# Performance work log

Measured on AMD Instinct MI355X. Metric: run time of the kernel, lower is better.

## Reference

```python
import jax, jax.numpy as jnp
import numpy as np

B = 1048576
EPS = 1e-5

def _lin_params(key, din, dout):
    k1, k2 = jax.random.split(key)
    bound = 1.0 / np.sqrt(din)
    w = jax.random.uniform(k1, (din, dout), minval=-bound, maxval=bound, dtype=jnp.float32)
    b = jax.random.uniform(k2, (dout,), minval=-bound, maxval=bound, dtype=jnp.float32)
    return w, b

def setup_inputs() -> dict:
    key = jax.random.key(0)
    ks = jax.random.split(key, 10)
    x = jax.random.normal(ks[0], (B, 8), dtype=jnp.float32)
    dims = [(8, 16), (16, 16), (16, 12), (12, 8), (8, 4), (4, 4), (4, 4), (4, 1)]
    names = ['fm', 'c1', 'p1', 'c2', 'p2', 'c3', 'r', 'h']
    inp = {'x': x,
           'bn_g': jnp.ones((8,), jnp.float32),
           'bn_b': jnp.zeros((8,), jnp.float32)}
    for i, (nm, (di, do)) in enumerate(zip(names, dims)):
        w, b = _lin_params(ks[i + 1], di, do)
        inp['w_' + nm] = w
        inp['b_' + nm] = b
    return inp

def reference(x, bn_g, bn_b, w_fm, b_fm, w_c1, b_c1, w_p1, b_p1, w_c2, b_c2,
              w_p2, b_p2, w_c3, b_c3, w_r, b_r, w_h, b_h):
    # BatchNorm1d (training mode): batch statistics, biased variance
    mu = jnp.mean(x, axis=0)
    var = jnp.mean((x - mu) ** 2, axis=0)
    h = (x - mu) * jax.lax.rsqrt(var + EPS) * bn_g + bn_b
    h = jnp.tanh(h @ w_fm + b_fm)   # [B,16] feature_map
    h = jnp.tanh(h @ w_c1 + b_c1)   # [B,16] conv1
    h = jnp.tanh(h @ w_p1 + b_p1)   # [B,12] pool1
    h = jnp.tanh(h @ w_c2 + b_c2)   # [B,8]  conv2
    h = jnp.tanh(h @ w_p2 + b_p2)   # [B,4]  pool2
    h = jnp.tanh(h @ w_c3 + b_c3)   # [B,4]  conv3
    res = jax.nn.relu(h @ w_r + b_r)  # [B,4] residual branch
    h = h + res
    return jax.nn.sigmoid(h @ w_h + b_h)  # [B,1]
```

## Files before the change

kernel.cpp:

```cpp
#include <hip/hip_runtime.h>
#include <stdint.h>

#define B_ROWS 1048576
#define STAT_BLOCKS 512
#define MAIN_BLOCKS 2048

typedef __fp16 h2 __attribute__((ext_vector_type(2)));

#define PART_OFF 16
#define WPK_OFF 8208
#define BIA_OFF 8578
#define W_FM 0
#define W_C1 64
#define W_P1 192
#define W_C2 288
#define W_P2 336
#define W_C3 352
#define W_R  360
#define W_H  368
#define B_FM 0
#define B_C1 16
#define B_P1 32
#define B_C2 44
#define B_P2 52
#define B_C3 56
#define B_R  60
#define B_H  64

__device__ __forceinline__ float exp_tanh(float x) {
    float e = __builtin_amdgcn_exp2f(x * 2.8853900817779268f);
    return 1.0f - 2.0f * __builtin_amdgcn_rcpf(e + 1.0f);
}

__device__ __forceinline__ float fast_sigmoid(float x) {
    float e = __builtin_amdgcn_exp2f(x * -1.4426950408889634f);
    return __builtin_amdgcn_rcpf(1.0f + e);
}

template<int DIN, int DOUT>
__device__ void pack_layer(const float* __restrict__ w, const float* __restrict__ b,
                           uint32_t* __restrict__ wdst, float* __restrict__ bdst) {
    for (int idx = threadIdx.x; idx < DOUT * (DIN / 2); idx += blockDim.x) {
        int j = idx / (DIN / 2), i2 = idx % (DIN / 2);
        h2 h;
        h.x = (__fp16)w[(2 * i2) * DOUT + j];
        h.y = (__fp16)w[(2 * i2 + 1) * DOUT + j];
        wdst[j * (DIN / 2) + i2] = __builtin_bit_cast(uint32_t, h);
    }
    for (int j = threadIdx.x; j < DOUT; j += blockDim.x) bdst[j] = b[j];
}

__global__ __launch_bounds__(256) void bn_stats(
    const float* __restrict__ x, float* __restrict__ ws,
    const float* __restrict__ w_fm, const float* __restrict__ b_fm,
    const float* __restrict__ w_c1, const float* __restrict__ b_c1,
    const float* __restrict__ w_p1, const float* __restrict__ b_p1,
    const float* __restrict__ w_c2, const float* __restrict__ b_c2,
    const float* __restrict__ w_p2, const float* __restrict__ b_p2,
    const float* __restrict__ w_c3, const float* __restrict__ b_c3,
    const float* __restrict__ w_r,  const float* __restrict__ b_r,
    const float* __restrict__ w_h,  const float* __restrict__ b_h)
{
    const int tid = blockIdx.x * 256 + threadIdx.x;
    float s[8], q[8];
#pragma unroll
    for (int c = 0; c < 8; ++c) { s[c] = 0.f; q[c] = 0.f; }
    const float4* x4 = (const float4*)x;
#pragma unroll
    for (int k = 0; k < 8; ++k) {
        int r = tid + k * 131072;
        float4 a = x4[2 * r];
        float4 b = x4[2 * r + 1];
        s[0] += a.x; s[1] += a.y; s[2] += a.z; s[3] += a.w;
        s[4] += b.x; s[5] += b.y; s[6] += b.z; s[7] += b.w;
        q[0] += a.x * a.x; q[1] += a.y * a.y; q[2] += a.z * a.z; q[3] += a.w * a.w;
        q[4] += b.x * b.x; q[5] += b.y * b.y; q[6] += b.z * b.z; q[7] += b.w * b.w;
    }
#pragma unroll
    for (int off = 32; off > 0; off >>= 1) {
#pragma unroll
        for (int c = 0; c < 8; ++c) {
            s[c] += __shfl_down(s[c], off);
            q[c] += __shfl_down(q[c], off);
        }
    }
    __shared__ float red[4][16];
    const int lane = threadIdx.x & 63;
    const int wave = threadIdx.x >> 6;
    if (lane == 0) {
#pragma unroll
        for (int c = 0; c < 8; ++c) { red[wave][c] = s[c]; red[wave][8 + c] = q[c]; }
    }
    __syncthreads();
    if (threadIdx.x < 16) {
        float acc = red[0][threadIdx.x] + red[1][threadIdx.x] +
                    red[2][threadIdx.x] + red[3][threadIdx.x];
        ws[PART_OFF + blockIdx.x * 16 + threadIdx.x] = acc;
    }
    if (blockIdx.x == 0) {
        uint32_t* wpk = (uint32_t*)(ws + WPK_OFF);
        float*    bpk = ws + BIA_OFF;
        pack_layer<8, 16>(w_fm, b_fm, wpk + W_FM, bpk + B_FM);
        pack_layer<16,16>(w_c1, b_c1, wpk + W_C1, bpk + B_C1);
        pack_layer<16,12>(w_p1, b_p1, wpk + W_P1, bpk + B_P1);
        pack_layer<12, 8>(w_c2, b_c2, wpk + W_C2, bpk + B_C2);
        pack_layer<8,  4>(w_p2, b_p2, wpk + W_P2, bpk + B_P2);
        pack_layer<4,  4>(w_c3, b_c3, wpk + W_C3, bpk + B_C3);
        pack_layer<4,  4>(w_r,  b_r,  wpk + W_R,  bpk + B_R);
        pack_layer<4,  1>(w_h,  b_h,  wpk + W_H,  bpk + B_H);
    }
}

__global__ __launch_bounds__(256) void bn_finalize(
    const float* __restrict__ bn_g, const float* __restrict__ bn_b,
    float* __restrict__ ws)
{
    __shared__ float accs[16][17];
    const int f = threadIdx.x & 15;
    const int chunk = threadIdx.x >> 4;
    const float* p = ws + PART_OFF + (chunk * 32) * 16 + f;
    float a = 0.f;
#pragma unroll 8
    for (int b = 0; b < 32; ++b) a += p[b * 16];
    accs[chunk][f] = a;
    __syncthreads();
    if (threadIdx.x < 16) {
        float t = 0.f;
#pragma unroll
        for (int c = 0; c < 16; ++c) t += accs[c][threadIdx.x];
        accs[0][threadIdx.x] = t;
    }
    __syncthreads();
    if (threadIdx.x < 8) {
        const float invB = 1.0f / (float)B_ROWS;
        int c = threadIdx.x;
        float mu  = accs[0][c] * invB;
        float var = fmaf(-mu, mu, accs[0][8 + c] * invB);
        float sv  = bn_g[c] * rsqrtf(var + 1e-5f);
        ws[c]     = sv;
        ws[8 + c] = fmaf(-mu, sv, bn_b[c]);
    }
}

__device__ __forceinline__ uint32_t lut_idx(float x) {
    float t = fmaf(x, 1024.0f, 4096.0f);
    t = __builtin_amdgcn_fmed3f(t, 0.0f, 8191.0f);
    return (uint32_t)t;
}

template<int DIN, int DOUT>
__device__ __forceinline__ void layer_dot1(const h2* __restrict__ apk,
                                           float* __restrict__ o,
                                           const uint32_t* __restrict__ wpk,
                                           const float* __restrict__ bias) {
#pragma unroll
    for (int j = 0; j < DOUT; ++j) {
        float acc = bias[j];
#pragma unroll
        for (int i2 = 0; i2 < DIN / 2; ++i2) {
            h2 w = __builtin_bit_cast(h2, wpk[j * (DIN / 2) + i2]);
            acc = __builtin_amdgcn_fdot2(apk[i2], w, acc, false);
        }
        o[j] = acc;
    }
}

template<int N>
__device__ __forceinline__ void tanh_pack1(const float* __restrict__ in,
                                           h2* __restrict__ pk,
                                           const uint16_t* __restrict__ lut16) {
#pragma unroll
    for (int k = 0; k < N / 2; ++k) {
        uint32_t v0 = lut16[lut_idx(in[2 * k])];
        uint32_t v1 = lut16[lut_idx(in[2 * k + 1])];
        pk[k] = __builtin_bit_cast(h2, v0 | (v1 << 16));
    }
}

__device__ __forceinline__ float row_forward(float4 x0, float4 x1,
        const float* __restrict__ sc, const float* __restrict__ sh,
        const uint32_t* __restrict__ wpk, const float* __restrict__ bpk,
        const uint16_t* __restrict__ lut16) {
    float n[8];
    n[0] = fmaf(x0.x, sc[0], sh[0]); n[1] = fmaf(x0.y, sc[1], sh[1]);
    n[2] = fmaf(x0.z, sc[2], sh[2]); n[3] = fmaf(x0.w, sc[3], sh[3]);
    n[4] = fmaf(x1.x, sc[4], sh[4]); n[5] = fmaf(x1.y, sc[5], sh[5]);
    n[6] = fmaf(x1.z, sc[6], sh[6]); n[7] = fmaf(x1.w, sc[7], sh[7]);
    h2 a[4];
#pragma unroll
    for (int k = 0; k < 4; ++k)
        a[k] = __builtin_amdgcn_cvt_pkrtz(n[2 * k], n[2 * k + 1]);

    float o1[16]; h2 p1[8];
    layer_dot1<8, 16>(a, o1, wpk + W_FM, bpk + B_FM);
    tanh_pack1<16>(o1, p1, lut16);
    float o2[16]; h2 p2[8];
    layer_dot1<16,16>(p1, o2, wpk + W_C1, bpk + B_C1);
    tanh_pack1<16>(o2, p2, lut16);
    float o3[12]; h2 p3[6];
    layer_dot1<16,12>(p2, o3, wpk + W_P1, bpk + B_P1);
    tanh_pack1<12>(o3, p3, lut16);
    float o4[8]; h2 p4[4];
    layer_dot1<12, 8>(p3, o4, wpk + W_C2, bpk + B_C2);
    tanh_pack1<8>(o4, p4, lut16);
    float o5[4]; h2 p5[2];
    layer_dot1<8,  4>(p4, o5, wpk + W_P2, bpk + B_P2);
    tanh_pack1<4>(o5, p5, lut16);
    float c4[4];
    layer_dot1<4,  4>(p5, c4, wpk + W_C3, bpk + B_C3);

    uint32_t u[4]; float f[4];
#pragma unroll
    for (int j = 0; j < 4; ++j) {
        u[j] = lut16[lut_idx(c4[j])];
        f[j] = (float)__builtin_bit_cast(__fp16, (uint16_t)u[j]);
    }
    h2 pc[2];
    pc[0] = __builtin_bit_cast(h2, u[0] | (u[1] << 16));
    pc[1] = __builtin_bit_cast(h2, u[2] | (u[3] << 16));
    float r4[4];
    layer_dot1<4,  4>(pc, r4, wpk + W_R, bpk + B_R);
#pragma unroll
    for (int j = 0; j < 4; ++j) f[j] += fmaxf(r4[j], 0.f);
    h2 ph[2];
    ph[0] = __builtin_amdgcn_cvt_pkrtz(f[0], f[1]);
    ph[1] = __builtin_amdgcn_cvt_pkrtz(f[2], f[3]);
    float oh[1];
    layer_dot1<4,  1>(ph, oh, wpk + W_H, bpk + B_H);
    return fast_sigmoid(oh[0]);
}

__global__ __launch_bounds__(256, 6) void qcnn_main(
    const float* __restrict__ x, const float* __restrict__ ws,
    float* __restrict__ out)
{
    const int tid = blockIdx.x * 256 + threadIdx.x;
    const int r0 = tid, r1 = tid + (B_ROWS / 2);
    const float4* x4 = (const float4*)x;
    float4 xa0 = x4[2 * r0], xa1 = x4[2 * r0 + 1];
    float4 xb0 = x4[2 * r1], xb1 = x4[2 * r1 + 1];

    __shared__ uint16_t lut16[8192];
    {
        const float h = 0.0009765625f;
        uint32_t* l32 = (uint32_t*)lut16;
#pragma unroll
        for (int k = 0; k < 16; ++k) {
            int i2 = threadIdx.x + k * 256;
            float c0 = fmaf((float)(2 * i2) + 0.5f, h, -4.0f);
            float c1 = fmaf((float)(2 * i2 + 1) + 0.5f, h, -4.0f);
            __fp16 h0 = (__fp16)exp_tanh(c0);
            __fp16 h1 = (__fp16)exp_tanh(c1);
            l32[i2] = (uint32_t)__builtin_bit_cast(uint16_t, h0)
                    | ((uint32_t)__builtin_bit_cast(uint16_t, h1) << 16);
        }
    }
    float sc[8], sh[8];
#pragma unroll
    for (int c = 0; c < 8; ++c) { sc[c] = ws[c]; sh[c] = ws[8 + c]; }
    __syncthreads();

    const uint32_t* wpk = (const uint32_t*)(ws + WPK_OFF);
    const float*    bpk = ws + BIA_OFF;

    out[r0] = row_forward(xa0, xa1, sc, sh, wpk, bpk, lut16);
    out[r1] = row_forward(xb0, xb1, sc, sh, wpk, bpk, lut16);
}

extern "C" void kernel_launch(void* const* d_in, const int* in_sizes, int n_in,
                              void* d_out, int out_size, void* d_ws, size_t ws_size,
                              hipStream_t stream) {
    const float* x    = (const float*)d_in[0];
    const float* bn_g = (const float*)d_in[1];
    const float* bn_b = (const float*)d_in[2];
    const float* w_fm = (const float*)d_in[3];
    const float* b_fm = (const float*)d_in[4];
    const float* w_c1 = (const float*)d_in[5];
    const float* b_c1 = (const float*)d_in[6];
    const float* w_p1 = (const float*)d_in[7];
    const float* b_p1 = (const float*)d_in[8];
    const float* w_c2 = (const float*)d_in[9];
    const float* b_c2 = (const float*)d_in[10];
    const float* w_p2 = (const float*)d_in[11];
    const float* b_p2 = (const float*)d_in[12];
    const float* w_c3 = (const float*)d_in[13];
    const float* b_c3 = (const float*)d_in[14];
    const float* w_r  = (const float*)d_in[15];
    const float* b_r  = (const float*)d_in[16];
    const float* w_h  = (const float*)d_in[17];
    const float* b_h  = (const float*)d_in[18];
    float* out = (float*)d_out;
    float* ws  = (float*)d_ws;

    bn_stats<<<STAT_BLOCKS, 256, 0, stream>>>(
        x, ws, w_fm, b_fm, w_c1, b_c1, w_p1, b_p1, w_c2, b_c2,
        w_p2, b_p2, w_c3, b_c3, w_r, b_r, w_h, b_h);
    bn_finalize<<<1, 256, 0, stream>>>(bn_g, bn_b, ws);
    qcnn_main<<<MAIN_BLOCKS, 256, 0, stream>>>(x, ws, out);
}
```

Before: 141.0 us.

## Fold batchnorm into first layer weights and replace tanh LUT with direct exp

Folds the batchnorm scale and shift into the first linear layer's packed fp16 weights and bias inside the finalize kernel, so the main kernel skips the per-row normalization FMAs. It also drops the 8192-entry shared-memory tanh lookup table, whose per-block construction, LDS use and syncthreads are removed, and computes tanh directly with exp_tanh plus packed conversion. This trades LDS gathers and table setup for more ALU transcendental work per activation, and raw x is now cast to fp16 before the scaled weights are applied, which changes rounding.

```diff
diff --git a/kernel.cpp b/kernel.cpp
--- a/kernel.cpp
+++ b/kernel.cpp
@@ -52,7 +52,6 @@
 
 __global__ __launch_bounds__(256) void bn_stats(
     const float* __restrict__ x, float* __restrict__ ws,
-    const float* __restrict__ w_fm, const float* __restrict__ b_fm,
     const float* __restrict__ w_c1, const float* __restrict__ b_c1,
     const float* __restrict__ w_p1, const float* __restrict__ b_p1,
     const float* __restrict__ w_c2, const float* __restrict__ b_c2,
@@ -100,7 +99,6 @@
     if (blockIdx.x == 0) {
         uint32_t* wpk = (uint32_t*)(ws + WPK_OFF);
         float*    bpk = ws + BIA_OFF;
-        pack_layer<8, 16>(w_fm, b_fm, wpk + W_FM, bpk + B_FM);
         pack_layer<16,16>(w_c1, b_c1, wpk + W_C1, bpk + B_C1);
         pack_layer<16,12>(w_p1, b_p1, wpk + W_P1, bpk + B_P1);
         pack_layer<12, 8>(w_c2, b_c2, wpk + W_C2, bpk + B_C2);
@@ -113,9 +111,11 @@
 
 __global__ __launch_bounds__(256) void bn_finalize(
     const float* __restrict__ bn_g, const float* __restrict__ bn_b,
+    const float* __restrict__ w_fm, const float* __restrict__ b_fm,
     float* __restrict__ ws)
 {
     __shared__ float accs[16][17];
+    __shared__ float scs[8], shs[8];
     const int f = threadIdx.x & 15;
     const int chunk = threadIdx.x >> 4;
     const float* p = ws + PART_OFF + (chunk * 32) * 16 + f;
@@ -137,15 +137,24 @@
         float mu  = accs[0][c] * invB;
         float var = fmaf(-mu, mu, accs[0][8 + c] * invB);
         float sv  = bn_g[c] * rsqrtf(var + 1e-5f);
-        ws[c]     = sv;
-        ws[8 + c] = fmaf(-mu, sv, bn_b[c]);
-    }
-}
-
-__device__ __forceinline__ uint32_t lut_idx(float x) {
-    float t = fmaf(x, 1024.0f, 4096.0f);
-    t = __builtin_amdgcn_fmed3f(t, 0.0f, 8191.0f);
-    return (uint32_t)t;
+        scs[c] = sv;
+        shs[c] = fmaf(-mu, sv, bn_b[c]);
+    }
+    __syncthreads();
+    if (threadIdx.x < 64) {
+        int j = threadIdx.x >> 2, i2 = threadIdx.x & 3;
+        h2 h;
+        h.x = (__fp16)(w_fm[(2 * i2) * 16 + j]     * scs[2 * i2]);
+        h.y = (__fp16)(w_fm[(2 * i2 + 1) * 16 + j] * scs[2 * i2 + 1]);
+        ((uint32_t*)(ws + WPK_OFF))[W_FM + j * 4 + i2] = __builtin_bit_cast(uint32_t, h);
+    }
+    if (threadIdx.x < 16) {
+        int j = threadIdx.x;
+        float acc = b_fm[j];
+#pragma unroll
+        for (int i = 0; i < 8; ++i) acc = fmaf(shs[i], w_fm[i * 16 + j], acc);
+        (ws + BIA_OFF)[B_FM + j] = acc;
+    }
 }
 
 template<int DIN, int DOUT>
@@ -167,57 +176,47 @@
 
 template<int N>
 __device__ __forceinline__ void tanh_pack1(const float* __restrict__ in,
-                                           h2* __restrict__ pk,
-                                           const uint16_t* __restrict__ lut16) {
+                                           h2* __restrict__ pk) {
 #pragma unroll
     for (int k = 0; k < N / 2; ++k) {
-        uint32_t v0 = lut16[lut_idx(in[2 * k])];
-        uint32_t v1 = lut16[lut_idx(in[2 * k + 1])];
-        pk[k] = __builtin_bit_cast(h2, v0 | (v1 << 16));
+        float t0 = exp_tanh(in[2 * k]);
+        float t1 = exp_tanh(in[2 * k + 1]);
+        pk[k] = __builtin_amdgcn_cvt_pkrtz(t0, t1);
     }
 }
 
 __device__ __forceinline__ float row_forward(float4 x0, float4 x1,
-        const float* __restrict__ sc, const float* __restrict__ sh,
-        const uint32_t* __restrict__ wpk, const float* __restrict__ bpk,
-        const uint16_t* __restrict__ lut16) {
-    float n[8];
-    n[0] = fmaf(x0.x, sc[0], sh[0]); n[1] = fmaf(x0.y, sc[1], sh[1]);
-    n[2] = fmaf(x0.z, sc[2], sh[2]); n[3] = fmaf(x0.w, sc[3], sh[3]);
-    n[4] = fmaf(x1.x, sc[4], sh[4]); n[5] = fmaf(x1.y, sc[5], sh[5]);
-    n[6] = fmaf(x1.z, sc[6], sh[6]); n[7] = fmaf(x1.w, sc[7], sh[7]);
+        const uint32_t* __restrict__ wpk, const float* __restrict__ bpk) {
     h2 a[4];
-#pragma unroll
-    for (int k = 0; k < 4; ++k)
-        a[k] = __builtin_amdgcn_cvt_pkrtz(n[2 * k], n[2 * k + 1]);
+    a[0] = __builtin_amdgcn_cvt_pkrtz(x0.x, x0.y);
+    a[1] = __builtin_amdgcn_cvt_pkrtz(x0.z, x0.w);
+    a[2] = __builtin_amdgcn_cvt_pkrtz(x1.x, x1.y);
+    a[3] = __builtin_amdgcn_cvt_pkrtz(x1.z, x1.w);
 
     float o1[16]; h2 p1[8];
     layer_dot1<8, 16>(a, o1, wpk + W_FM, bpk + B_FM);
-    tanh_pack1<16>(o1, p1, lut16);
+    tanh_pack1<16>(o1, p1);
     float o2[16]; h2 p2[8];
     layer_dot1<16,16>(p1, o2, wpk + W_C1, bpk + B_C1);
-    tanh_pack1<16>(o2, p2, lut16);
+    tanh_pack1<16>(o2, p2);
     float o3[12]; h2 p3[6];
     layer_dot1<16,12>(p2, o3, wpk + W_P1, bpk + B_P1);
-    tanh_pack1<12>(o3, p3, lut16);
+    tanh_pack1<12>(o3, p3);
     float o4[8]; h2 p4[4];
     layer_dot1<12, 8>(p3, o4, wpk + W_C2, bpk + B_C2);
-    tanh_pack1<8>(o4, p4, lut16);
+    tanh_pack1<8>(o4, p4);
     float o5[4]; h2 p5[2];
     layer_dot1<8,  4>(p4, o5, wpk + W_P2, bpk + B_P2);
-    tanh_pack1<4>(o5, p5, lut16);
+    tanh_pack1<4>(o5, p5);
     float c4[4];
     layer_dot1<4,  4>(p5, c4, wpk + W_C3, bpk + B_C3);
 
-    uint32_t u[4]; float f[4];
-#pragma unroll
-    for (int j = 0; j < 4; ++j) {
-        u[j] = lut16[lut_idx(c4[j])];
-        f[j] = (float)__builtin_bit_cast(__fp16, (uint16_t)u[j]);
-    }
+    float f[4];
+#pragma unroll
+    for (int j = 0; j < 4; ++j) f[j] = exp_tanh(c4[j]);
     h2 pc[2];
-    pc[0] = __builtin_bit_cast(h2, u[0] | (u[1] << 16));
-    pc[1] = __builtin_bit_cast(h2, u[2] | (u[3] << 16));
+    pc[0] = __builtin_amdgcn_cvt_pkrtz(f[0], f[1]);
+    pc[1] = __builtin_amdgcn_cvt_pkrtz(f[2], f[3]);
     float r4[4];
     layer_dot1<4,  4>(pc, r4, wpk + W_R, bpk + B_R);
 #pragma unroll
@@ -240,31 +239,11 @@
     float4 xa0 = x4[2 * r0], xa1 = x4[2 * r0 + 1];
     float4 xb0 = x4[2 * r1], xb1 = x4[2 * r1 + 1];
 
-    __shared__ uint16_t lut16[8192];
-    {
-        const float h = 0.0009765625f;
-        uint32_t* l32 = (uint32_t*)lut16;
-#pragma unroll
-        for (int k = 0; k < 16; ++k) {
-            int i2 = threadIdx.x + k * 256;
-            float c0 = fmaf((float)(2 * i2) + 0.5f, h, -4.0f);
-            float c1 = fmaf((float)(2 * i2 + 1) + 0.5f, h, -4.0f);
-            __fp16 h0 = (__fp16)exp_tanh(c0);
-            __fp16 h1 = (__fp16)exp_tanh(c1);
-            l32[i2] = (uint32_t)__builtin_bit_cast(uint16_t, h0)
-                    | ((uint32_t)__builtin_bit_cast(uint16_t, h1) << 16);
-        }
-    }
-    float sc[8], sh[8];
-#pragma unroll
-    for (int c = 0; c < 8; ++c) { sc[c] = ws[c]; sh[c] = ws[8 + c]; }
-    __syncthreads();
-
     const uint32_t* wpk = (const uint32_t*)(ws + WPK_OFF);
     const float*    bpk = ws + BIA_OFF;
 
-    out[r0] = row_forward(xa0, xa1, sc, sh, wpk, bpk, lut16);
-    out[r1] = row_forward(xb0, xb1, sc, sh, wpk, bpk, lut16);
+    out[r0] = row_forward(xa0, xa1, wpk, bpk);
+    out[r1] = row_forward(xb0, xb1, wpk, bpk);
 }
 
 extern "C" void kernel_launch(void* const* d_in, const int* in_sizes, int n_in,
@@ -293,8 +272,8 @@
     float* ws  = (float*)d_ws;
 
     bn_stats<<<STAT_BLOCKS, 256, 0, stream>>>(
-        x, ws, w_fm, b_fm, w_c1, b_c1, w_p1, b_p1, w_c2, b_c2,
+        x, ws, w_c1, b_c1, w_p1, b_p1, w_c2, b_c2,
         w_p2, b_p2, w_c3, b_c3, w_r, b_r, w_h, b_h);
-    bn_finalize<<<1, 256, 0, stream>>>(bn_g, bn_b, ws);
+    bn_finalize<<<1, 256, 0, stream>>>(bn_g, bn_b, w_fm, b_fm, ws);
     qcnn_main<<<MAIN_BLOCKS, 256, 0, stream>>>(x, ws, out);
 }
```

After: 139.2 us. Within noise of the previous version (-1.3%).
